# Performance work log

Measured on AMD Instinct MI355X. Metric: run time of the kernel, lower is better.

## Reference

```python
import jax, jax.numpy as jnp
import numpy as np

B, S, H = 64, 4096, 256

def setup_inputs() -> dict:
    key = jax.random.key(0)
    k1, k2, k3, k4, k5 = jax.random.split(key, 5)
    scale = 1.0 / np.sqrt(H)
    return {
        "query": jax.random.normal(k1, (B, H), dtype=jnp.float32),
        "keys": jax.random.normal(k2, (B, S, H), dtype=jnp.float32),
        "Wq": jax.random.normal(k3, (H, H), dtype=jnp.float32) * scale,
        "Wk": jax.random.normal(k4, (H, H), dtype=jnp.float32) * scale,
        "V": jax.random.normal(k5, (H,), dtype=jnp.float32) * scale,
    }

def reference(query, keys, Wq, Wk, V):
    # q_proj: [B,1,H], k_proj: [B,S,H]
    q_proj = (query @ Wq.T)[:, None, :]
    k_proj = jnp.einsum('bsh,gh->bsg', keys, Wk)
    scores = jnp.einsum('bsh,h->bs', jnp.tanh(q_proj + k_proj), V)  # [B,S]
    weights = jax.nn.softmax(scores, axis=-1)
    context = jnp.einsum('bs,bsh->bh', weights, keys)
    return (context, weights)
```

## Files before the change

### kernel.cpp

```cpp
#include <hip/hip_runtime.h>
#include <hip/hip_bf16.h>

#define B 64
#define S 4096
#define H 256
#define BM 128
#define BK 32

typedef short bf16x8 __attribute__((ext_vector_type(8)));
typedef float f32x4 __attribute__((ext_vector_type(4)));

__global__ __launch_bounds__(256) void wk_split(const float* __restrict__ Wk,
                                                unsigned short* __restrict__ WkHi,
                                                unsigned short* __restrict__ WkLo) {
    int i = (blockIdx.x * 256 + threadIdx.x) * 4;
    float4 x = *(const float4*)(Wk + i);
    float f[4] = {x.x, x.y, x.z, x.w};
    unsigned int hw[2], lw[2];
    #pragma unroll
    for (int j = 0; j < 2; ++j) {
        unsigned int u0 = __float_as_uint(f[2 * j]);
        unsigned int u1 = __float_as_uint(f[2 * j + 1]);
        float h0 = __uint_as_float(u0 & 0xFFFF0000u);
        float h1 = __uint_as_float(u1 & 0xFFFF0000u);
        unsigned int l0 = __float_as_uint(f[2 * j] - h0) >> 16;
        unsigned int l1 = __float_as_uint(f[2 * j + 1] - h1) >> 16;
        hw[j] = (u0 >> 16) | (u1 & 0xFFFF0000u);
        lw[j] = l0 | (l1 << 16);
    }
    *(uint2*)(WkHi + i) = make_uint2(hw[0], hw[1]);
    *(uint2*)(WkLo + i) = make_uint2(lw[0], lw[1]);
}

__global__ __launch_bounds__(256) void qproj_kernel(const float* __restrict__ query,
                                                    const float* __restrict__ Wq,
                                                    float* __restrict__ qp) {
    int b = blockIdx.x, h = threadIdx.x;
    __shared__ float qrow[H];
    qrow[h] = query[b * H + h];
    __syncthreads();
    const float* wrow = Wq + h * H;
    float acc = 0.f;
    #pragma unroll 8
    for (int g = 0; g < H; g += 4) {
        float4 w = *(const float4*)(wrow + g);
        acc += w.x * qrow[g] + w.y * qrow[g + 1] + w.z * qrow[g + 2] + w.w * qrow[g + 3];
    }
    qp[b * H + h] = acc;
}

__global__ __launch_bounds__(512) void scores_kernel(
    const float* __restrict__ keys,
    const unsigned short* __restrict__ WkHi,
    const unsigned short* __restrict__ WkLo,
    const float* __restrict__ qp,
    const float* __restrict__ V,
    float* __restrict__ scores)
{
    __shared__ unsigned short Ahi[BM][40], Alo[BM][40];
    __shared__ unsigned short Bhi[H][40], Blo[H][40];
    __shared__ float part[4][BM];

    const int b  = blockIdx.y;
    const int s0 = blockIdx.x * BM;
    const int tid  = threadIdx.x;
    const int lane = tid & 63;
    const int wid  = tid >> 6;
    const int lr = lane & 15, lg = lane >> 4;
    const int mg = wid >> 2, ng = wid & 3;

    const int ar = tid >> 2;
    const int ak = (tid & 3) * 8;
    const int br = tid >> 1;
    const int bk = (tid & 1) * 16;

    const float* aptr = keys + ((size_t)(b * S + s0 + ar)) * H + ak;
    const unsigned short* bhptr = WkHi + br * H + bk;
    const unsigned short* blptr = WkLo + br * H + bk;

    f32x4 acc[4][4];
    #pragma unroll
    for (int mi = 0; mi < 4; ++mi)
        #pragma unroll
        for (int ni = 0; ni < 4; ++ni) acc[mi][ni] = (f32x4){0.f, 0.f, 0.f, 0.f};

    float qv[4], vv[4];
    #pragma unroll
    for (int ni = 0; ni < 4; ++ni) {
        int c = ng * 64 + ni * 16 + lr;
        qv[ni] = qp[b * H + c];
        vv[ni] = V[c];
    }

    float4 a0 = *(const float4*)(aptr);
    float4 a1 = *(const float4*)(aptr + 4);
    uint4 bh0 = *(const uint4*)(bhptr);
    uint4 bh1 = *(const uint4*)(bhptr + 8);
    uint4 bl0 = *(const uint4*)(blptr);
    uint4 bl1 = *(const uint4*)(blptr + 8);

    for (int t = 0; t < 8; ++t) {
        float f[8] = {a0.x, a0.y, a0.z, a0.w, a1.x, a1.y, a1.z, a1.w};
        unsigned int hw[4], lw[4];
        #pragma unroll
        for (int j = 0; j < 4; ++j) {
            unsigned int u0 = __float_as_uint(f[2 * j]);
            unsigned int u1 = __float_as_uint(f[2 * j + 1]);
            float h0 = __uint_as_float(u0 & 0xFFFF0000u);
            float h1 = __uint_as_float(u1 & 0xFFFF0000u);
            unsigned int l0 = __float_as_uint(f[2 * j] - h0) >> 16;
            unsigned int l1 = __float_as_uint(f[2 * j + 1] - h1) >> 16;
            hw[j] = (u0 >> 16) | (u1 & 0xFFFF0000u);
            lw[j] = l0 | (l1 << 16);
        }
        *(uint4*)&Ahi[ar][ak] = make_uint4(hw[0], hw[1], hw[2], hw[3]);
        *(uint4*)&Alo[ar][ak] = make_uint4(lw[0], lw[1], lw[2], lw[3]);
        *(uint4*)&Bhi[br][bk] = bh0;
        *(uint4*)&Bhi[br][bk + 8] = bh1;
        *(uint4*)&Blo[br][bk] = bl0;
        *(uint4*)&Blo[br][bk + 8] = bl1;

        if (t < 7) {
            int k1 = (t + 1) * BK;
            a0 = *(const float4*)(aptr + k1);
            a1 = *(const float4*)(aptr + k1 + 4);
            bh0 = *(const uint4*)(bhptr + k1);
            bh1 = *(const uint4*)(bhptr + k1 + 8);
            bl0 = *(const uint4*)(blptr + k1);
            bl1 = *(const uint4*)(blptr + k1 + 8);
        }
        __syncthreads();

        bf16x8 bhf[4], blf[4];
        #pragma unroll
        for (int ni = 0; ni < 4; ++ni) {
            bhf[ni] = *(const bf16x8*)&Bhi[ng * 64 + ni * 16 + lr][lg * 8];
            blf[ni] = *(const bf16x8*)&Blo[ng * 64 + ni * 16 + lr][lg * 8];
        }
        #pragma unroll
        for (int mi = 0; mi < 4; ++mi) {
            bf16x8 ah = *(const bf16x8*)&Ahi[mg * 64 + mi * 16 + lr][lg * 8];
            bf16x8 al = *(const bf16x8*)&Alo[mg * 64 + mi * 16 + lr][lg * 8];
            #pragma unroll
            for (int ni = 0; ni < 4; ++ni) {
                acc[mi][ni] = __builtin_amdgcn_mfma_f32_16x16x32_bf16(ah, bhf[ni], acc[mi][ni], 0, 0, 0);
                acc[mi][ni] = __builtin_amdgcn_mfma_f32_16x16x32_bf16(ah, blf[ni], acc[mi][ni], 0, 0, 0);
                acc[mi][ni] = __builtin_amdgcn_mfma_f32_16x16x32_bf16(al, bhf[ni], acc[mi][ni], 0, 0, 0);
            }
        }
        __syncthreads();
    }

    #pragma unroll
    for (int mi = 0; mi < 4; ++mi) {
        #pragma unroll
        for (int r = 0; r < 4; ++r) {
            float p = 0.f;
            #pragma unroll
            for (int ni = 0; ni < 4; ++ni) {
                float x = qv[ni] + acc[mi][ni][r];
                float e = __expf(2.f * x);
                float tnh = 1.f - 2.f / (e + 1.f);
                p += vv[ni] * tnh;
            }
            p += __shfl_xor(p, 1);
            p += __shfl_xor(p, 2);
            p += __shfl_xor(p, 4);
            p += __shfl_xor(p, 8);
            if (lr == 0) part[ng][mg * 64 + mi * 16 + lg * 4 + r] = p;
        }
    }
    __syncthreads();
    if (tid < BM) {
        float sc = part[0][tid] + part[1][tid] + part[2][tid] + part[3][tid];
        scores[(size_t)b * S + s0 + tid] = sc;
    }
}

__global__ __launch_bounds__(1024) void softmax_kernel(const float* __restrict__ scores,
                                                       float* __restrict__ weights) {
    __shared__ float red[16];
    int b = blockIdx.x, tid = threadIdx.x;
    int lane = tid & 63, wid = tid >> 6;
    const float* src = scores + (size_t)b * S;

    float4 v = *(const float4*)(src + tid * 4);
    float m = fmaxf(fmaxf(v.x, v.y), fmaxf(v.z, v.w));
    #pragma unroll
    for (int off = 32; off; off >>= 1) m = fmaxf(m, __shfl_xor(m, off));
    if (lane == 0) red[wid] = m;
    __syncthreads();
    float M = red[0];
    #pragma unroll
    for (int i = 1; i < 16; ++i) M = fmaxf(M, red[i]);
    __syncthreads();

    v.x = __expf(v.x - M);
    v.y = __expf(v.y - M);
    v.z = __expf(v.z - M);
    v.w = __expf(v.w - M);
    float sum = v.x + v.y + v.z + v.w;
    #pragma unroll
    for (int off = 32; off; off >>= 1) sum += __shfl_xor(sum, off);
    if (lane == 0) red[wid] = sum;
    __syncthreads();
    float tot = 0.f;
    #pragma unroll
    for (int i = 0; i < 16; ++i) tot += red[i];
    float inv = 1.f / tot;

    v.x *= inv; v.y *= inv; v.z *= inv; v.w *= inv;
    *(float4*)(weights + (size_t)b * S + tid * 4) = v;
}

__global__ __launch_bounds__(256) void context_kernel(const float* __restrict__ keys,
                                                      const float* __restrict__ weights,
                                                      float* __restrict__ ctx) {
    int b = blockIdx.y, chunk = blockIdx.x, tid = threadIdx.x;
    __shared__ float w[128];
    if (tid < 128) w[tid] = weights[(size_t)b * S + chunk * 128 + tid];
    __syncthreads();

    int sl = tid >> 6;
    int h4 = (tid & 63) * 4;
    float4 acc = {0.f, 0.f, 0.f, 0.f};
    const float* kb = keys + ((size_t)(b * S + chunk * 128)) * H;
    #pragma unroll 4
    for (int s = sl; s < 128; s += 4) {
        float ws = w[s];
        float4 k4 = *(const float4*)(kb + (size_t)s * H + h4);
        acc.x += ws * k4.x;
        acc.y += ws * k4.y;
        acc.z += ws * k4.z;
        acc.w += ws * k4.w;
    }

    __shared__ float4 partc[4][64];
    partc[sl][tid & 63] = acc;
    __syncthreads();
    if (sl == 0) {
        float4 t = partc[0][tid];
        #pragma unroll
        for (int g = 1; g < 4; ++g) {
            float4 p = partc[g][tid];
            t.x += p.x; t.y += p.y; t.z += p.z; t.w += p.w;
        }
        atomicAdd(&ctx[b * H + h4 + 0], t.x);
        atomicAdd(&ctx[b * H + h4 + 1], t.y);
        atomicAdd(&ctx[b * H + h4 + 2], t.z);
        atomicAdd(&ctx[b * H + h4 + 3], t.w);
    }
}

extern "C" void kernel_launch(void* const* d_in, const int* in_sizes, int n_in,
                              void* d_out, int out_size, void* d_ws, size_t ws_size,
                              hipStream_t stream) {
    const float* query = (const float*)d_in[0];
    const float* keys  = (const float*)d_in[1];
    const float* Wq    = (const float*)d_in[2];
    const float* Wk    = (const float*)d_in[3];
    const float* V     = (const float*)d_in[4];

    float* ctx     = (float*)d_out;
    float* weights = (float*)d_out + B * H;

    float* qp            = (float*)d_ws;
    unsigned short* WkHi = (unsigned short*)(qp + B * H);
    unsigned short* WkLo = WkHi + H * H;
    float* scoresBuf     = (float*)(WkLo + H * H);

    hipMemsetAsync(ctx, 0, B * H * sizeof(float), stream);
    wk_split<<<64, 256, 0, stream>>>(Wk, WkHi, WkLo);
    qproj_kernel<<<B, 256, 0, stream>>>(query, Wq, qp);
    scores_kernel<<<dim3(S / BM, B), 512, 0, stream>>>(keys, WkHi, WkLo, qp, V, scoresBuf);
    softmax_kernel<<<B, 1024, 0, stream>>>(scoresBuf, weights);
    context_kernel<<<dim3(32, B), 256, 0, stream>>>(keys, weights, ctx);
}
```

Baseline: 531.4 us.

## Deepen key prefetch in scores GEMM and replace atomic context reduction

The scores kernel now prefetches the keys tile two K-steps ahead with double register buffers, fully unrolls the K loop, replaces __syncthreads with raw s_barrier plus an explicit lgkmcnt wait and sched barriers, and adds a minimum-occupancy launch bound. The context stage drops the memset and float atomics in favour of per-chunk partial writes followed by a separate reduction kernel. The aim is to hide global load latency in the memory-bound GEMM and avoid atomic contention. In exchange it uses more registers, risks spills under the occupancy bound, and adds an extra kernel launch plus a partial buffer in the workspace.

```diff
diff --git a/kernel.cpp b/kernel.cpp
--- a/kernel.cpp
+++ b/kernel.cpp
@@ -49,7 +49,7 @@
     qp[b * H + h] = acc;
 }
 
-__global__ __launch_bounds__(512) void scores_kernel(
+__global__ __launch_bounds__(512, 4) void scores_kernel(
     const float* __restrict__ keys,
     const unsigned short* __restrict__ WkHi,
     const unsigned short* __restrict__ WkLo,
@@ -92,44 +92,65 @@
         vv[ni] = V[c];
     }
 
-    float4 a0 = *(const float4*)(aptr);
-    float4 a1 = *(const float4*)(aptr + 4);
-    uint4 bh0 = *(const uint4*)(bhptr);
-    uint4 bh1 = *(const uint4*)(bhptr + 8);
-    uint4 bl0 = *(const uint4*)(blptr);
-    uint4 bl1 = *(const uint4*)(blptr + 8);
-
+    uint4 bp0, bp1, bp2, bp3;
+    float4 a0A, a1A, a0B, a1B;
+    bp0 = *(const uint4*)(bhptr);
+    bp1 = *(const uint4*)(bhptr + 8);
+    bp2 = *(const uint4*)(blptr);
+    bp3 = *(const uint4*)(blptr + 8);
+    a0A = *(const float4*)(aptr);
+    a1A = *(const float4*)(aptr + 4);
+    a0B = *(const float4*)(aptr + BK);
+    a1B = *(const float4*)(aptr + BK + 4);
+
+    #pragma unroll
     for (int t = 0; t < 8; ++t) {
-        float f[8] = {a0.x, a0.y, a0.z, a0.w, a1.x, a1.y, a1.z, a1.w};
-        unsigned int hw[4], lw[4];
-        #pragma unroll
-        for (int j = 0; j < 4; ++j) {
-            unsigned int u0 = __float_as_uint(f[2 * j]);
-            unsigned int u1 = __float_as_uint(f[2 * j + 1]);
-            float h0 = __uint_as_float(u0 & 0xFFFF0000u);
-            float h1 = __uint_as_float(u1 & 0xFFFF0000u);
-            unsigned int l0 = __float_as_uint(f[2 * j] - h0) >> 16;
-            unsigned int l1 = __float_as_uint(f[2 * j + 1] - h1) >> 16;
-            hw[j] = (u0 >> 16) | (u1 & 0xFFFF0000u);
-            lw[j] = l0 | (l1 << 16);
-        }
-        *(uint4*)&Ahi[ar][ak] = make_uint4(hw[0], hw[1], hw[2], hw[3]);
-        *(uint4*)&Alo[ar][ak] = make_uint4(lw[0], lw[1], lw[2], lw[3]);
-        *(uint4*)&Bhi[br][bk] = bh0;
-        *(uint4*)&Bhi[br][bk + 8] = bh1;
-        *(uint4*)&Blo[br][bk] = bl0;
-        *(uint4*)&Blo[br][bk + 8] = bl1;
+        float4 a0 = (t & 1) ? a0B : a0A;
+        float4 a1 = (t & 1) ? a1B : a1A;
+        {
+            float f[8] = {a0.x, a0.y, a0.z, a0.w, a1.x, a1.y, a1.z, a1.w};
+            unsigned int hw[4], lw[4];
+            #pragma unroll
+            for (int j = 0; j < 4; ++j) {
+                unsigned int u0 = __float_as_uint(f[2 * j]);
+                unsigned int u1 = __float_as_uint(f[2 * j + 1]);
+                float h0 = __uint_as_float(u0 & 0xFFFF0000u);
+                float h1 = __uint_as_float(u1 & 0xFFFF0000u);
+                unsigned int l0 = __float_as_uint(f[2 * j] - h0) >> 16;
+                unsigned int l1 = __float_as_uint(f[2 * j + 1] - h1) >> 16;
+                hw[j] = (u0 >> 16) | (u1 & 0xFFFF0000u);
+                lw[j] = l0 | (l1 << 16);
+            }
+            *(uint4*)&Ahi[ar][ak] = make_uint4(hw[0], hw[1], hw[2], hw[3]);
+            *(uint4*)&Alo[ar][ak] = make_uint4(lw[0], lw[1], lw[2], lw[3]);
+        }
+        *(uint4*)&Bhi[br][bk] = bp0;
+        *(uint4*)&Bhi[br][bk + 8] = bp1;
+        *(uint4*)&Blo[br][bk] = bp2;
+        *(uint4*)&Blo[br][bk + 8] = bp3;
 
         if (t < 7) {
             int k1 = (t + 1) * BK;
-            a0 = *(const float4*)(aptr + k1);
-            a1 = *(const float4*)(aptr + k1 + 4);
-            bh0 = *(const uint4*)(bhptr + k1);
-            bh1 = *(const uint4*)(bhptr + k1 + 8);
-            bl0 = *(const uint4*)(blptr + k1);
-            bl1 = *(const uint4*)(blptr + k1 + 8);
-        }
-        __syncthreads();
+            bp0 = *(const uint4*)(bhptr + k1);
+            bp1 = *(const uint4*)(bhptr + k1 + 8);
+            bp2 = *(const uint4*)(blptr + k1);
+            bp3 = *(const uint4*)(blptr + k1 + 8);
+        }
+        if (t < 6) {
+            int k2 = (t + 2) * BK;
+            if (t & 1) {
+                a0B = *(const float4*)(aptr + k2);
+                a1B = *(const float4*)(aptr + k2 + 4);
+            } else {
+                a0A = *(const float4*)(aptr + k2);
+                a1A = *(const float4*)(aptr + k2 + 4);
+            }
+        }
+
+        __builtin_amdgcn_sched_barrier(0);
+        asm volatile("s_waitcnt lgkmcnt(0)" ::: "memory");
+        __builtin_amdgcn_s_barrier();
+        __builtin_amdgcn_sched_barrier(0);
 
         bf16x8 bhf[4], blf[4];
         #pragma unroll
@@ -148,7 +169,9 @@
                 acc[mi][ni] = __builtin_amdgcn_mfma_f32_16x16x32_bf16(al, bhf[ni], acc[mi][ni], 0, 0, 0);
             }
         }
-        __syncthreads();
+
+        __builtin_amdgcn_sched_barrier(0);
+        __builtin_amdgcn_s_barrier();
     }
 
     #pragma unroll
@@ -213,9 +236,9 @@
     *(float4*)(weights + (size_t)b * S + tid * 4) = v;
 }
 
-__global__ __launch_bounds__(256) void context_kernel(const float* __restrict__ keys,
-                                                      const float* __restrict__ weights,
-                                                      float* __restrict__ ctx) {
+__global__ __launch_bounds__(256) void context_partial(const float* __restrict__ keys,
+                                                       const float* __restrict__ weights,
+                                                       float* __restrict__ partial) {
     int b = blockIdx.y, chunk = blockIdx.x, tid = threadIdx.x;
     __shared__ float w[128];
     if (tid < 128) w[tid] = weights[(size_t)b * S + chunk * 128 + tid];
@@ -245,11 +268,17 @@
             float4 p = partc[g][tid];
             t.x += p.x; t.y += p.y; t.z += p.z; t.w += p.w;
         }
-        atomicAdd(&ctx[b * H + h4 + 0], t.x);
-        atomicAdd(&ctx[b * H + h4 + 1], t.y);
-        atomicAdd(&ctx[b * H + h4 + 2], t.z);
-        atomicAdd(&ctx[b * H + h4 + 3], t.w);
-    }
+        *(float4*)&partial[((size_t)chunk * B + b) * H + h4] = t;
+    }
+}
+
+__global__ __launch_bounds__(256) void ctx_reduce(const float* __restrict__ partial,
+                                                  float* __restrict__ ctx) {
+    int b = blockIdx.x, h = threadIdx.x;
+    float s = 0.f;
+    #pragma unroll
+    for (int c = 0; c < 32; ++c) s += partial[((size_t)c * B + b) * H + h];
+    ctx[b * H + h] = s;
 }
 
 extern "C" void kernel_launch(void* const* d_in, const int* in_sizes, int n_in,
@@ -268,11 +297,12 @@
     unsigned short* WkHi = (unsigned short*)(qp + B * H);
     unsigned short* WkLo = WkHi + H * H;
     float* scoresBuf     = (float*)(WkLo + H * H);
-
-    hipMemsetAsync(ctx, 0, B * H * sizeof(float), stream);
+    float* partial       = scoresBuf + (size_t)B * S;
+
     wk_split<<<64, 256, 0, stream>>>(Wk, WkHi, WkLo);
     qproj_kernel<<<B, 256, 0, stream>>>(query, Wq, qp);
     scores_kernel<<<dim3(S / BM, B), 512, 0, stream>>>(keys, WkHi, WkLo, qp, V, scoresBuf);
     softmax_kernel<<<B, 1024, 0, stream>>>(scoresBuf, weights);
-    context_kernel<<<dim3(32, B), 256, 0, stream>>>(keys, weights, ctx);
-}
+    context_partial<<<dim3(32, B), 256, 0, stream>>>(keys, weights, partial);
+    ctx_reduce<<<B, 256, 0, stream>>>(partial, ctx);
+}
```

Measured after the change: 879.7 us. 1.66x slower.
